# Kernel tuning notes

Hardware: AMD Instinct MI355X
Metric: run time of the kernel (lower is better)

## Reference

```python
import jax, jax.numpy as jnp
import numpy as np

N = 50000      # nodes
E = 800000     # edges (avg degree 16)
F_IN = 128
H = 128        # hidden_channels
C = 10         # num_classes
S = 5          # Chebyshev order K
B = 8          # graphs in batch


def setup_inputs() -> dict:
    key = jax.random.key(0)
    ks = jax.random.split(key, 9)
    x = jax.random.normal(ks[0], (N, F_IN), jnp.float32)
    edge_index = jax.random.randint(ks[1], (2, E), 0, N, dtype=jnp.int64)
    batch = jnp.sort(jax.random.randint(ks[2], (N,), 0, B, dtype=jnp.int64))
    lambda_max = 2.0 * jnp.ones((B,), jnp.float32)
    W1 = jax.random.normal(ks[3], (S, F_IN, H), jnp.float32) * 0.05
    b1 = jax.random.normal(ks[4], (H,), jnp.float32) * 0.05
    W2 = jax.random.normal(ks[5], (S, H, H), jnp.float32) * 0.05
    b2 = jax.random.normal(ks[6], (H,), jnp.float32) * 0.05
    Wlin = jax.random.normal(ks[7], (H, C), jnp.float32) * 0.05
    blin = jax.random.normal(ks[8], (C,), jnp.float32) * 0.05
    return {"x": x, "edge_index": edge_index, "batch": batch,
            "lambda_max": lambda_max, "W1": W1, "b1": b1,
            "W2": W2, "b2": b2, "Wlin": Wlin, "blin": blin}


def _cheb_conv(x, row, col, w_edge, diag, W, b):
    # scaled Laplacian matvec: L_hat v = scatter(w_edge * v[col] -> row) + diag * v
    def Lhat(v):
        msg = v[col] * w_edge[:, None]                       # [E, d]
        return jax.ops.segment_sum(msg, row, num_segments=N) + diag[:, None] * v

    Tx0 = x
    out = Tx0 @ W[0]
    Tx1 = Lhat(Tx0)
    out = out + Tx1 @ W[1]
    for k in range(2, W.shape[0]):                           # Chebyshev recurrence
        Tx2 = 2.0 * Lhat(Tx1) - Tx0
        out = out + Tx2 @ W[k]
        Tx0, Tx1 = Tx1, Tx2
    return out + b


def reference(x, edge_index, batch, lambda_max, W1, b1, W2, b2, Wlin, blin):
    row, col = edge_index[0], edge_index[1]
    # sym-normalized Laplacian L = I - D^{-1/2} A D^{-1/2}; L_hat = 2L/lambda_max - I
    deg = jax.ops.segment_sum(jnp.ones((E,), x.dtype), row, num_segments=N)
    dis = jnp.where(deg > 0, jax.lax.rsqrt(jnp.maximum(deg, 1e-12)), 0.0)
    lam_e = lambda_max[batch[row]]                           # per-edge lambda_max
    w_edge = -2.0 * dis[row] * dis[col] / lam_e              # off-diagonal of L_hat
    diag = 2.0 / lambda_max[batch] - 1.0                     # diagonal of L_hat per node

    h = jax.nn.relu(_cheb_conv(x, row, col, w_edge, diag, W1, b1))
    h = jax.nn.relu(_cheb_conv(h, row, col, w_edge, diag, W2, b2))

    # global_mean_pool over batch assignment
    sums = jax.ops.segment_sum(h, batch, num_segments=B)     # [B, H]
    counts = jax.ops.segment_sum(jnp.ones((N, 1), h.dtype), batch, num_segments=B)
    pooled = sums / jnp.maximum(counts, 1.0)
    return pooled @ Wlin + blin                              # [B, C] logits (softmax unused in forward)
```

## Files before the change

kernel.cpp:

```cpp
#include <hip/hip_runtime.h>
#include <hip/hip_bf16.h>
#include <stdint.h>

typedef __attribute__((ext_vector_type(8))) short bf16x8;
typedef __attribute__((ext_vector_type(4))) float f32x4;

__device__ __forceinline__ float bf16lo_to_f(uint32_t u) { return __uint_as_float(u << 16); }
__device__ __forceinline__ float bf16hi_to_f(uint32_t u) { return __uint_as_float(u & 0xffff0000u); }
__device__ __forceinline__ uint16_t f_to_bf16(float f) {
    uint32_t u = __float_as_uint(f);
    uint32_t r = u + 0x7fff + ((u >> 16) & 1);
    return (uint16_t)(r >> 16);
}


#define BINCH 4096

__global__ void __launch_bounds__(256) k_bhist(const int* __restrict__ row,
                                               int* __restrict__ bhist, int E) {
    __shared__ int sh[256];
    int t = threadIdx.x;
    sh[t] = 0;
    __syncthreads();
    int stride = gridDim.x * blockDim.x;
    for (int e = blockIdx.x * blockDim.x + t; e < E; e += stride)
        atomicAdd(&sh[row[e] >> 8], 1);
    __syncthreads();
    if (sh[t]) atomicAdd(&bhist[t], sh[t]);
}

__global__ void k_bscan(const int* __restrict__ bhist, int* __restrict__ gbase,
                        int* __restrict__ gcur, int nbk) {
    __shared__ int sh[256];
    int t = threadIdx.x;
    int v = t < nbk ? bhist[t] : 0;
    sh[t] = v;
    __syncthreads();
    for (int o = 1; o < 256; o <<= 1) {
        int u = (t >= o) ? sh[t - o] : 0;
        __syncthreads();
        sh[t] += u;
        __syncthreads();
    }
    gbase[t] = sh[t] - v;
    gcur[t] = sh[t] - v;
    if (t == 255) gbase[256] = sh[255];
}

__global__ void __launch_bounds__(256) k_bin(const int* __restrict__ row,
        const int* __restrict__ col, int* __restrict__ gcur,
        uint32_t* __restrict__ bout, int E) {
    __shared__ uint32_t stage[BINCH];
    __shared__ int hist[256], hscan[256], hcur[256], gofs[256];
    int t = threadIdx.x;
    int e0 = blockIdx.x * BINCH;
    int ecnt = min(BINCH, E - e0);
    hist[t] = 0;
    __syncthreads();
    for (int i = t; i < ecnt; i += 256)
        atomicAdd(&hist[row[e0 + i] >> 8], 1);
    __syncthreads();
    int v = hist[t];
    hscan[t] = v;
    __syncthreads();
    for (int o = 1; o < 256; o <<= 1) {
        int u = (t >= o) ? hscan[t - o] : 0;
        __syncthreads();
        hscan[t] += u;
        __syncthreads();
    }
    hcur[t] = hscan[t] - v;
    __syncthreads();
    for (int i = t; i < ecnt; i += 256) {
        int r = row[e0 + i];
        int p = atomicAdd(&hcur[r >> 8], 1);
        stage[p] = (uint32_t)(r & 255) | ((uint32_t)col[e0 + i] << 8);
    }
    __syncthreads();
    if (v > 0) gofs[t] = atomicAdd(&gcur[t], v);
    __syncthreads();
    for (int i = t; i < ecnt; i += 256) {
        int lo = 0, hi = 255;
        while (lo < hi) { int mid = (lo + hi) >> 1; if (hscan[mid] > i) hi = mid; else lo = mid + 1; }
        int b = lo;
        int local = i - (hscan[b] - hist[b]);
        bout[gofs[b] + local] = stage[i];
    }
}

__global__ void __launch_bounds__(256) k_deg2(const uint32_t* __restrict__ bout,
        const int* __restrict__ gbase, int* __restrict__ deg, int N) {
    __shared__ int cnt[256];
    int t = threadIdx.x, b = blockIdx.x;
    cnt[t] = 0;
    __syncthreads();
    int s = gbase[b], epos = gbase[b + 1];
    for (int i = s + t; i < epos; i += 256)
        atomicAdd(&cnt[bout[i] & 255], 1);
    __syncthreads();
    int n = b * 256 + t;
    if (n < N) deg[n] = cnt[t];
}

__global__ void k_psum(const int* __restrict__ deg, int* __restrict__ psum, int N) {
    __shared__ int sh[256];
    int t = threadIdx.x;
    int idx = blockIdx.x * 256 + t;
    sh[t] = idx < N ? ((deg[idx] + 7) & ~7) : 0;
    __syncthreads();
    for (int o = 128; o > 0; o >>= 1) {
        if (t < o) sh[t] += sh[t + o];
        __syncthreads();
    }
    if (t == 0) psum[blockIdx.x] = sh[0];
}

__global__ void k_scanp(const int* __restrict__ psum, int* __restrict__ poff,
                        int* __restrict__ offs, int nb, int N) {
    __shared__ int sh[256];
    int t = threadIdx.x;
    int per = (nb + 255) >> 8;
    int base = t * per;
    int s = 0;
    for (int i = 0; i < per; i++) { int idx = base + i; if (idx < nb) s += psum[idx]; }
    sh[t] = s;
    __syncthreads();
    for (int o = 1; o < 256; o <<= 1) {
        int u = (t >= o) ? sh[t - o] : 0;
        __syncthreads();
        sh[t] += u;
        __syncthreads();
    }
    int run = sh[t] - s;
    for (int i = 0; i < per; i++) {
        int idx = base + i;
        if (idx < nb) { poff[idx] = run; run += psum[idx]; }
    }
    if (t == 255) offs[N] = sh[255];
}

__global__ void k_offs(const int* __restrict__ deg, const int* __restrict__ poff,
                       int* __restrict__ offs,
                       const int* __restrict__ batch, const float* __restrict__ lam,
                       float* __restrict__ dis, float* __restrict__ diag, int N) {
    __shared__ int sh[256];
    int t = threadIdx.x;
    int idx = blockIdx.x * 256 + t;
    int d = idx < N ? deg[idx] : 0;
    int v = (d + 7) & ~7;
    sh[t] = v;
    __syncthreads();
    for (int o = 1; o < 256; o <<= 1) {
        int u = (t >= o) ? sh[t - o] : 0;
        __syncthreads();
        sh[t] += u;
        __syncthreads();
    }
    if (idx < N) {
        offs[idx] = poff[blockIdx.x] + sh[t] - v;
        dis[idx] = d > 0 ? rsqrtf((float)d) : 0.f;
        diag[idx] = 2.f / lam[batch[idx]] - 1.f;
    }
}

__global__ void __launch_bounds__(256) k_csr2(const uint32_t* __restrict__ bout,
        const int* __restrict__ gbase, const int* __restrict__ offs,
        uint16_t* __restrict__ csr, int N) {
    __shared__ int cur[256];
    int t = threadIdx.x, b = blockIdx.x;
    int n = b * 256 + t;
    cur[t] = n < N ? offs[n] : 0;
    __syncthreads();
    int s = gbase[b], epos = gbase[b + 1];
    for (int i = s + t; i < epos; i += 256) {
        uint32_t v = bout[i];
        int p = atomicAdd(&cur[v & 255], 1);
        csr[p] = (uint16_t)(v >> 8);
    }
}

__global__ void k_prepw(const float* __restrict__ W1, uint16_t* __restrict__ Wt1,
                        const float* __restrict__ W2, uint16_t* __restrict__ Wt2) {
    int i = blockIdx.x * blockDim.x + threadIdx.x;
    const float* W = W1; uint16_t* Wt = Wt1;
    if (i >= 128 * 640) { i -= 128 * 640; W = W2; Wt = Wt2; }
    int o = i / 640, kk = i % 640;
    Wt[(size_t)o * 640 + kk] = f_to_bf16(W[(size_t)kk * 128 + o]);
}

__global__ void __launch_bounds__(256) k_castx(const float* __restrict__ x,
        uint16_t* __restrict__ Txb, int8_t* __restrict__ Txq,
        const float* __restrict__ dis, float* __restrict__ mS, int N) {
    int n = (blockIdx.x * blockDim.x + threadIdx.x) >> 6;
    int lane = threadIdx.x & 63;
    if (n >= N) return;
    float2 v = ((const float2*)x)[(size_t)n * 64 + lane];
    uint32_t p = (uint32_t)f_to_bf16(v.x) | ((uint32_t)f_to_bf16(v.y) << 16);
    ((uint32_t*)Txb)[(size_t)n * 320 + lane] = p;
    float m = fmaxf(fabsf(v.x), fabsf(v.y));
    for (int o = 1; o < 64; o <<= 1) m = fmaxf(m, __shfl_xor(m, o));
    float inv = m > 0.f ? 127.f / m : 0.f;
    int qx = (int)rintf(v.x * inv), qy = (int)rintf(v.y * inv);
    uint16_t qp = (uint16_t)((qx & 0xff) | ((qy & 0xff) << 8));
    *(uint16_t*)(Txq + (size_t)n * 640 + 2 * lane) = qp;
    if (lane == 0) mS[n] = (m > 0.f ? m * (1.f / 127.f) : 0.f) * dis[n];
}

__global__ void __launch_bounds__(256) k_lhat(
        int8_t* __restrict__ Txq, uint16_t* __restrict__ Txb,
        const int* __restrict__ offs, const uint16_t* __restrict__ csr,
        const float* __restrict__ diag, const float* __restrict__ dis,
        float* __restrict__ mS, int N,
        int src, int dst, int prev, float alpha, int use_prev) {
    int n = (blockIdx.x * blockDim.x + threadIdx.x) >> 6;
    int lane = threadIdx.x & 63;
    if (n >= N) return;
    int beg = offs[n], end = offs[n + 1];
    float dgn = diag[n], dn = dis[n];
    float aS = -alpha * dn * (dgn + 1.0f);
    const float* mSrc = mS + (size_t)src * (N + 1);
    const int8_t* qbase = Txq + src * 128 + 2 * lane;
    float ax = 0.f, ay = 0.f;
    for (int e = beg; e < end; e += 8) {
        uint4 cw = *(const uint4*)(csr + e);
        int cc[8] = { (int)(cw.x & 0xffff), (int)(cw.x >> 16),
                      (int)(cw.y & 0xffff), (int)(cw.y >> 16),
                      (int)(cw.z & 0xffff), (int)(cw.z >> 16),
                      (int)(cw.w & 0xffff), (int)(cw.w >> 16) };
        float mm[8];
        uint16_t qv[8];
#pragma unroll
        for (int u = 0; u < 8; u++) mm[u] = mSrc[cc[u]];
#pragma unroll
        for (int u = 0; u < 8; u++)
            qv[u] = *(const uint16_t*)(qbase + (size_t)cc[u] * 640);
#pragma unroll
        for (int u = 0; u < 8; u++) {
            float f = aS * mm[u];
            ax = fmaf(f, (float)(int)(int8_t)(qv[u] & 0xff), ax);
            ay = fmaf(f, (float)(int)(int8_t)(qv[u] >> 8), ay);
        }
    }
    const uint32_t* bb = (const uint32_t*)Txb;
    uint32_t sv = bb[(size_t)n * 320 + src * 64 + lane];
    float ad = alpha * dgn;
    ax += ad * bf16lo_to_f(sv);
    ay += ad * bf16hi_to_f(sv);
    if (use_prev) {
        uint32_t pv = bb[(size_t)n * 320 + prev * 64 + lane];
        ax -= bf16lo_to_f(pv);
        ay -= bf16hi_to_f(pv);
    }
    uint32_t outv = (uint32_t)f_to_bf16(ax) | ((uint32_t)f_to_bf16(ay) << 16);
    ((uint32_t*)Txb)[(size_t)n * 320 + dst * 64 + lane] = outv;
    float m = fmaxf(fabsf(ax), fabsf(ay));
    for (int o = 1; o < 64; o <<= 1) m = fmaxf(m, __shfl_xor(m, o));
    float inv = m > 0.f ? 127.f / m : 0.f;
    int qx = (int)rintf(ax * inv), qy = (int)rintf(ay * inv);
    uint16_t qp = (uint16_t)((qx & 0xff) | ((qy & 0xff) << 8));
    *(uint16_t*)(Txq + (size_t)n * 640 + dst * 128 + 2 * lane) = qp;
    if (lane == 0)
        mS[(size_t)dst * (N + 1) + n] = (m > 0.f ? m * (1.f / 127.f) : 0.f) * dn;
}

#define BM 128
#define BK 64
#define LDT 72
#define LDC 132

__global__ void __launch_bounds__(256) k_gemm(
        const uint16_t* __restrict__ A, int lda,
        const uint16_t* __restrict__ Bt,
        const float* __restrict__ bias,
        uint16_t* __restrict__ out, int ldo,
        uint16_t* __restrict__ out2b,
        int8_t* __restrict__ out2q,
        const float* __restrict__ dis, float* __restrict__ mS,
        int M, int Kdim) {
    __shared__ uint16_t smem[BM * LDT + 128 * LDT];
    uint16_t* As = smem;
    uint16_t* Bs = smem + BM * LDT;
    uint16_t* Ct = smem;
    int t = threadIdx.x;
    int w = t >> 6, lane = t & 63;
    int row0 = blockIdx.x * BM;
    int mrow = (w >> 1) * 64, ncol = (w & 1) * 64;

    int ar[4], akc[4];
#pragma unroll
    for (int rep = 0; rep < 4; rep++) {
        int d = rep * 256 + t;
        ar[rep] = d >> 3; akc[rep] = d & 7;
    }

    f32x4 acc[4][4];
#pragma unroll
    for (int i = 0; i < 4; i++)
#pragma unroll
        for (int j = 0; j < 4; j++) acc[i][j] = (f32x4){0.f, 0.f, 0.f, 0.f};

    bf16x8 pa[4], pb[4];
#pragma unroll
    for (int rep = 0; rep < 4; rep++) {
        int grow = row0 + ar[rep];
        bf16x8 va = {0, 0, 0, 0, 0, 0, 0, 0};
        if (grow < M) va = *(const bf16x8*)(A + (size_t)grow * lda + akc[rep] * 8);
        pa[rep] = va;
        pb[rep] = *(const bf16x8*)(Bt + (size_t)ar[rep] * Kdim + akc[rep] * 8);
    }

    for (int k0 = 0; k0 < Kdim; k0 += BK) {
#pragma unroll
        for (int rep = 0; rep < 4; rep++) {
            *(bf16x8*)(&As[ar[rep] * LDT + akc[rep] * 8]) = pa[rep];
            *(bf16x8*)(&Bs[ar[rep] * LDT + akc[rep] * 8]) = pb[rep];
        }
        __syncthreads();
        int kn = k0 + BK;
        if (kn < Kdim) {
#pragma unroll
            for (int rep = 0; rep < 4; rep++) {
                int grow = row0 + ar[rep];
                bf16x8 va = {0, 0, 0, 0, 0, 0, 0, 0};
                if (grow < M) va = *(const bf16x8*)(A + (size_t)grow * lda + kn + akc[rep] * 8);
                pa[rep] = va;
                pb[rep] = *(const bf16x8*)(Bt + (size_t)ar[rep] * Kdim + kn + akc[rep] * 8);
            }
        }
#pragma unroll
        for (int ks = 0; ks < BK; ks += 32) {
            bf16x8 af[4], bfr[4];
#pragma unroll
            for (int i = 0; i < 4; i++) {
                int r = mrow + i * 16 + (lane & 15);
                af[i] = *(const bf16x8*)(&As[r * LDT + ks + (lane >> 4) * 8]);
            }
#pragma unroll
            for (int j = 0; j < 4; j++) {
                int c = ncol + j * 16 + (lane & 15);
                bfr[j] = *(const bf16x8*)(&Bs[c * LDT + ks + (lane >> 4) * 8]);
            }
#pragma unroll
            for (int i = 0; i < 4; i++)
#pragma unroll
                for (int j = 0; j < 4; j++)
                    acc[i][j] = __builtin_amdgcn_mfma_f32_16x16x32_bf16(af[i], bfr[j], acc[i][j], 0, 0, 0);
        }
        __syncthreads();
    }

#pragma unroll
    for (int j = 0; j < 4; j++) {
        int c = ncol + j * 16 + (lane & 15);
        float bv = bias[c];
#pragma unroll
        for (int i = 0; i < 4; i++) {
            int rloc = mrow + i * 16 + (lane >> 4) * 4;
#pragma unroll
            for (int r = 0; r < 4; r++) {
                float v = acc[i][j][r] + bv;
                v = v > 0.f ? v : 0.f;
                Ct[(rloc + r) * LDC + c] = f_to_bf16(v);
            }
        }
    }
    __syncthreads();
#pragma unroll
    for (int rep = 0; rep < 8; rep++) {
        int d = rep * 256 + t;
        int r = d >> 4, c8 = (d & 15) * 8;
        int grow = row0 + r;
        if (grow < M) {
            bf16x8 v = *(const bf16x8*)(&Ct[r * LDC + c8]);
            *(bf16x8*)(out + (size_t)grow * ldo + c8) = v;
            if (out2b) *(bf16x8*)(out2b + (size_t)grow * 640 + c8) = v;
        }
    }
    if (out2q) {
        int r = t >> 1, half = t & 1;
        int grow = row0 + r;
        float vmax = 0.f;
        for (int j = 0; j < 32; j++) {
            uint32_t u = *(const uint32_t*)(&Ct[r * LDC + half * 64 + j * 2]);
            vmax = fmaxf(vmax, fmaxf(fabsf(bf16lo_to_f(u)), fabsf(bf16hi_to_f(u))));
        }
        vmax = fmaxf(vmax, __shfl_xor(vmax, 1));
        if (grow < M) {
            float inv = vmax > 0.f ? 127.f / vmax : 0.f;
            for (int j0 = 0; j0 < 16; j0++) {
                uint32_t u0 = *(const uint32_t*)(&Ct[r * LDC + half * 64 + j0 * 4]);
                uint32_t u1 = *(const uint32_t*)(&Ct[r * LDC + half * 64 + j0 * 4 + 2]);
                int q0 = (int)rintf(bf16lo_to_f(u0) * inv);
                int q1 = (int)rintf(bf16hi_to_f(u0) * inv);
                int q2 = (int)rintf(bf16lo_to_f(u1) * inv);
                int q3 = (int)rintf(bf16hi_to_f(u1) * inv);
                uint32_t pk = (q0 & 0xff) | ((q1 & 0xff) << 8) |
                              ((q2 & 0xff) << 16) | ((uint32_t)(q3 & 0xff) << 24);
                *(uint32_t*)(out2q + (size_t)grow * 640 + half * 64 + j0 * 4) = pk;
            }
            if (half == 0)
                mS[grow] = (vmax > 0.f ? vmax * (1.f / 127.f) : 0.f) * dis[grow];
        }
    }
}

__global__ void __launch_bounds__(128) k_pool(const uint16_t* __restrict__ h,
        const int* __restrict__ batch, float* __restrict__ pooled, int N, int CH) {
    int f = threadIdx.x;
    int n0 = blockIdx.x * CH;
    if (n0 >= N) return;
    int n1 = min(n0 + CH, N);
    float acc = 0.f;
    int cur = batch[n0];
    for (int n = n0; n < n1; ++n) {
        int b = batch[n];
        if (b != cur) { atomicAdd(&pooled[cur * 128 + f], acc); acc = 0.f; cur = b; }
        acc += __uint_as_float(((uint32_t)h[(size_t)n * 128 + f]) << 16);
    }
    atomicAdd(&pooled[cur * 128 + f], acc);
}

__global__ void k_final(const float* __restrict__ pooled, const int* __restrict__ batch,
                        const float* __restrict__ Wlin, const float* __restrict__ blin,
                        float* __restrict__ out, int N, int B_, int C_) {
    __shared__ int cnt[64];
    int t = threadIdx.x;
    if (t < B_) {
        auto lb = [&](int v) {
            int lo = 0, hi = N;
            while (lo < hi) {
                int mid = (lo + hi) >> 1;
                if (batch[mid] < v) lo = mid + 1; else hi = mid;
            }
            return lo;
        };
        cnt[t] = lb(t + 1) - lb(t);
    }
    __syncthreads();
    if (t < B_ * C_) {
        int b = t / C_, c = t % C_;
        float inv = 1.f / fmaxf((float)cnt[b], 1.f);
        float acc = blin[c];
        for (int f = 0; f < 128; ++f) acc += pooled[b * 128 + f] * inv * Wlin[f * C_ + c];
        out[t] = acc;
    }
}

extern "C" void kernel_launch(void* const* d_in, const int* in_sizes, int n_in,
                              void* d_out, int out_size, void* d_ws, size_t ws_size,
                              hipStream_t stream) {
    const float* x    = (const float*)d_in[0];
    const int*   edge = (const int*)d_in[1];
    const int*   batch= (const int*)d_in[2];
    const float* lam  = (const float*)d_in[3];
    const float* W1   = (const float*)d_in[4];
    const float* b1   = (const float*)d_in[5];
    const float* W2   = (const float*)d_in[6];
    const float* b2   = (const float*)d_in[7];
    const float* Wlin = (const float*)d_in[8];
    const float* blin = (const float*)d_in[9];
    const int E  = in_sizes[1] / 2;
    const int N  = in_sizes[2];
    const int B_ = in_sizes[3];
    const int* row = edge;
    const int* col = edge + E;

    char* ws = (char*)d_ws;
    size_t off = 0;
    auto take = [&](size_t bytes) -> char* {
        char* p = ws + off;
        off = (off + bytes + 255) & ~(size_t)255;
        return p;
    };
    uint16_t* Txb    = (uint16_t*)take((size_t)N * 640 * 2);
    int8_t*   Txq    = (int8_t*)take((size_t)(N + 1) * 640);
    uint16_t* h      = (uint16_t*)take((size_t)N * 128 * 2);
    uint16_t* csr    = (uint16_t*)take(((size_t)E + 8 * (size_t)N) * 2);
    uint32_t* bout   = (uint32_t*)take((size_t)E * 4);
    float*    mS     = (float*)take((size_t)5 * (N + 1) * 4);
    int*      deg    = (int*)take((size_t)N * 4);
    int*      offs   = (int*)take((size_t)(N + 1) * 4);
    float*    dis    = (float*)take((size_t)N * 4);
    float*    diag   = (float*)take((size_t)N * 4);
    uint16_t* Wt1    = (uint16_t*)take((size_t)128 * 640 * 2);
    uint16_t* Wt2    = (uint16_t*)take((size_t)128 * 640 * 2);
    float*    pooled = (float*)take((size_t)B_ * 128 * 4);
    int*      bhist  = (int*)take(257 * 4);
    int*      gbase  = (int*)take(257 * 4);
    int*      gcur   = (int*)take(257 * 4);
    const int nb = (N + 255) / 256;
    int*      psum   = (int*)take((size_t)nb * 4);
    int*      poff   = (int*)take((size_t)nb * 4);

    hipMemsetAsync(pooled, 0, (size_t)B_ * 128 * 4, stream);
    hipMemsetAsync(mS, 0, (size_t)5 * (N + 1) * 4, stream);
    hipMemsetAsync(bhist, 0, 257 * 4, stream);
    hipMemsetD16Async((hipDeviceptr_t)csr, (unsigned short)N,
                      (size_t)E + 8 * (size_t)N, stream);

    k_bhist<<<112, 256, 0, stream>>>(row, bhist, E);
    k_bscan<<<1, 256, 0, stream>>>(bhist, gbase, gcur, nb);
    k_bin<<<(E + BINCH - 1) / BINCH, 256, 0, stream>>>(row, col, gcur, bout, E);
    k_deg2<<<nb, 256, 0, stream>>>(bout, gbase, deg, N);
    k_psum<<<nb, 256, 0, stream>>>(deg, psum, N);
    k_scanp<<<1, 256, 0, stream>>>(psum, poff, offs, nb, N);
    k_offs<<<nb, 256, 0, stream>>>(deg, poff, offs, batch, lam, dis, diag, N);
    k_csr2<<<nb, 256, 0, stream>>>(bout, gbase, offs, csr, N);
    k_prepw<<<(2 * 128 * 640) / 256, 256, 0, stream>>>(W1, Wt1, W2, Wt2);
    k_castx<<<(N + 3) / 4, 256, 0, stream>>>(x, Txb, Txq, dis, mS, N);

    const int lblocks = (N + 3) / 4;
    const int gblocks = (N + BM - 1) / BM;

    k_lhat<<<lblocks, 256, 0, stream>>>(Txq, Txb, offs, csr, diag, dis, mS, N, 0, 1, 0, 1.f, 0);
    k_lhat<<<lblocks, 256, 0, stream>>>(Txq, Txb, offs, csr, diag, dis, mS, N, 1, 2, 0, 2.f, 1);
    k_lhat<<<lblocks, 256, 0, stream>>>(Txq, Txb, offs, csr, diag, dis, mS, N, 2, 3, 1, 2.f, 1);
    k_lhat<<<lblocks, 256, 0, stream>>>(Txq, Txb, offs, csr, diag, dis, mS, N, 3, 4, 2, 2.f, 1);
    k_gemm<<<gblocks, 256, 0, stream>>>(Txb, 640, Wt1, b1, h, 128, Txb, Txq, dis, mS, N, 640);

    k_lhat<<<lblocks, 256, 0, stream>>>(Txq, Txb, offs, csr, diag, dis, mS, N, 0, 1, 0, 1.f, 0);
    k_lhat<<<lblocks, 256, 0, stream>>>(Txq, Txb, offs, csr, diag, dis, mS, N, 1, 2, 0, 2.f, 1);
    k_lhat<<<lblocks, 256, 0, stream>>>(Txq, Txb, offs, csr, diag, dis, mS, N, 2, 3, 1, 2.f, 1);
    k_lhat<<<lblocks, 256, 0, stream>>>(Txq, Txb, offs, csr, diag, dis, mS, N, 3, 4, 2, 2.f, 1);
    k_gemm<<<gblocks, 256, 0, stream>>>(Txb, 640, Wt2, b2, h, 128,
                                        (uint16_t*)nullptr, (int8_t*)nullptr, dis, mS, N, 640);

    k_pool<<<(N + 127) / 128, 128, 0, stream>>>(h, batch, pooled, N, 128);
    k_final<<<1, 128, 0, stream>>>(pooled, batch, Wlin, blin, (float*)d_out, N, B_, 10);
}
```

Measured before the change: 513.7 us.

## Cut memsets and bf16 reads in lhat, fuse degree/psum, pad CSR in-kernel

Removes the full mS and CSR memsets: only the dummy-node entries of mS are zeroed in the scan kernel, and CSR padding slots are filled by k_csr2 after its scatter. Fuses the per-block padded-degree reduction into k_deg2, dropping a launch. k_lhat now reads its self and previous Chebyshev terms from the int8 copy with a stored per-node scale instead of the bf16 copy, and writes bf16 outputs with nontemporal stores. The first GEMM no longer writes the unused h output. The int8 self/prev terms add quantization error to the recurrence, and scq is an extra per-node array.

```diff
diff --git a/kernel.cpp b/kernel.cpp
--- a/kernel.cpp
+++ b/kernel.cpp
@@ -30,7 +30,7 @@
 }
 
 __global__ void k_bscan(const int* __restrict__ bhist, int* __restrict__ gbase,
-                        int* __restrict__ gcur, int nbk) {
+                        int* __restrict__ gcur, float* __restrict__ mS, int nbk, int N) {
     __shared__ int sh[256];
     int t = threadIdx.x;
     int v = t < nbk ? bhist[t] : 0;
@@ -45,6 +45,7 @@
     gbase[t] = sh[t] - v;
     gcur[t] = sh[t] - v;
     if (t == 255) gbase[256] = sh[255];
+    if (t < 5) mS[(size_t)t * (N + 1) + N] = 0.f;
 }
 
 __global__ void __launch_bounds__(256) k_bin(const int* __restrict__ row,
@@ -89,8 +90,10 @@
 }
 
 __global__ void __launch_bounds__(256) k_deg2(const uint32_t* __restrict__ bout,
-        const int* __restrict__ gbase, int* __restrict__ deg, int N) {
+        const int* __restrict__ gbase, int* __restrict__ deg,
+        int* __restrict__ psum, int N) {
     __shared__ int cnt[256];
+    __shared__ int red[256];
     int t = threadIdx.x, b = blockIdx.x;
     cnt[t] = 0;
     __syncthreads();
@@ -99,20 +102,15 @@
         atomicAdd(&cnt[bout[i] & 255], 1);
     __syncthreads();
     int n = b * 256 + t;
-    if (n < N) deg[n] = cnt[t];
-}
-
-__global__ void k_psum(const int* __restrict__ deg, int* __restrict__ psum, int N) {
-    __shared__ int sh[256];
-    int t = threadIdx.x;
-    int idx = blockIdx.x * 256 + t;
-    sh[t] = idx < N ? ((deg[idx] + 7) & ~7) : 0;
+    int d = cnt[t];
+    if (n < N) deg[n] = d;
+    red[t] = (n < N) ? ((d + 7) & ~7) : 0;
     __syncthreads();
     for (int o = 128; o > 0; o >>= 1) {
-        if (t < o) sh[t] += sh[t + o];
-        __syncthreads();
-    }
-    if (t == 0) psum[blockIdx.x] = sh[0];
+        if (t < o) red[t] += red[t + o];
+        __syncthreads();
+    }
+    if (t == 0) psum[b] = red[0];
 }
 
 __global__ void k_scanp(const int* __restrict__ psum, int* __restrict__ poff,
@@ -169,13 +167,20 @@
     __shared__ int cur[256];
     int t = threadIdx.x, b = blockIdx.x;
     int n = b * 256 + t;
-    cur[t] = n < N ? offs[n] : 0;
+    int o0 = n < N ? offs[n] : 0;
+    cur[t] = o0;
     __syncthreads();
     int s = gbase[b], epos = gbase[b + 1];
     for (int i = s + t; i < epos; i += 256) {
         uint32_t v = bout[i];
         int p = atomicAdd(&cur[v & 255], 1);
         csr[p] = (uint16_t)(v >> 8);
+    }
+    __syncthreads();
+    if (n < N) {
+        int e = cur[t];
+        int pe = o0 + ((e - o0 + 7) & ~7);
+        for (int p = e; p < pe; p++) csr[p] = (uint16_t)N;
     }
 }
 
@@ -190,27 +195,32 @@
 
 __global__ void __launch_bounds__(256) k_castx(const float* __restrict__ x,
         uint16_t* __restrict__ Txb, int8_t* __restrict__ Txq,
-        const float* __restrict__ dis, float* __restrict__ mS, int N) {
+        const float* __restrict__ dis, float* __restrict__ mS,
+        float* __restrict__ scq, int N) {
     int n = (blockIdx.x * blockDim.x + threadIdx.x) >> 6;
     int lane = threadIdx.x & 63;
     if (n >= N) return;
     float2 v = ((const float2*)x)[(size_t)n * 64 + lane];
     uint32_t p = (uint32_t)f_to_bf16(v.x) | ((uint32_t)f_to_bf16(v.y) << 16);
-    ((uint32_t*)Txb)[(size_t)n * 320 + lane] = p;
+    __builtin_nontemporal_store(p, &((uint32_t*)Txb)[(size_t)n * 320 + lane]);
     float m = fmaxf(fabsf(v.x), fabsf(v.y));
     for (int o = 1; o < 64; o <<= 1) m = fmaxf(m, __shfl_xor(m, o));
     float inv = m > 0.f ? 127.f / m : 0.f;
     int qx = (int)rintf(v.x * inv), qy = (int)rintf(v.y * inv);
     uint16_t qp = (uint16_t)((qx & 0xff) | ((qy & 0xff) << 8));
     *(uint16_t*)(Txq + (size_t)n * 640 + 2 * lane) = qp;
-    if (lane == 0) mS[n] = (m > 0.f ? m * (1.f / 127.f) : 0.f) * dis[n];
+    if (lane == 0) {
+        float sc = m > 0.f ? m * (1.f / 127.f) : 0.f;
+        mS[n] = sc * dis[n];
+        scq[n] = sc;
+    }
 }
 
 __global__ void __launch_bounds__(256) k_lhat(
         int8_t* __restrict__ Txq, uint16_t* __restrict__ Txb,
         const int* __restrict__ offs, const uint16_t* __restrict__ csr,
         const float* __restrict__ diag, const float* __restrict__ dis,
-        float* __restrict__ mS, int N,
+        float* __restrict__ mS, float* __restrict__ scq, int N,
         int src, int dst, int prev, float alpha, int use_prev) {
     int n = (blockIdx.x * blockDim.x + threadIdx.x) >> 6;
     int lane = threadIdx.x & 63;
@@ -241,26 +251,31 @@
             ay = fmaf(f, (float)(int)(int8_t)(qv[u] >> 8), ay);
         }
     }
-    const uint32_t* bb = (const uint32_t*)Txb;
-    uint32_t sv = bb[(size_t)n * 320 + src * 64 + lane];
-    float ad = alpha * dgn;
-    ax += ad * bf16lo_to_f(sv);
-    ay += ad * bf16hi_to_f(sv);
+    {
+        uint16_t qsv = *(const uint16_t*)(Txq + (size_t)n * 640 + src * 128 + 2 * lane);
+        float ad = alpha * dgn * scq[(size_t)src * (N + 1) + n];
+        ax = fmaf(ad, (float)(int)(int8_t)(qsv & 0xff), ax);
+        ay = fmaf(ad, (float)(int)(int8_t)(qsv >> 8), ay);
+    }
     if (use_prev) {
-        uint32_t pv = bb[(size_t)n * 320 + prev * 64 + lane];
-        ax -= bf16lo_to_f(pv);
-        ay -= bf16hi_to_f(pv);
+        uint16_t qpv = *(const uint16_t*)(Txq + (size_t)n * 640 + prev * 128 + 2 * lane);
+        float sp = scq[(size_t)prev * (N + 1) + n];
+        ax = fmaf(-sp, (float)(int)(int8_t)(qpv & 0xff), ax);
+        ay = fmaf(-sp, (float)(int)(int8_t)(qpv >> 8), ay);
     }
     uint32_t outv = (uint32_t)f_to_bf16(ax) | ((uint32_t)f_to_bf16(ay) << 16);
-    ((uint32_t*)Txb)[(size_t)n * 320 + dst * 64 + lane] = outv;
+    __builtin_nontemporal_store(outv, &((uint32_t*)Txb)[(size_t)n * 320 + dst * 64 + lane]);
     float m = fmaxf(fabsf(ax), fabsf(ay));
     for (int o = 1; o < 64; o <<= 1) m = fmaxf(m, __shfl_xor(m, o));
     float inv = m > 0.f ? 127.f / m : 0.f;
     int qx = (int)rintf(ax * inv), qy = (int)rintf(ay * inv);
     uint16_t qp = (uint16_t)((qx & 0xff) | ((qy & 0xff) << 8));
     *(uint16_t*)(Txq + (size_t)n * 640 + dst * 128 + 2 * lane) = qp;
-    if (lane == 0)
-        mS[(size_t)dst * (N + 1) + n] = (m > 0.f ? m * (1.f / 127.f) : 0.f) * dn;
+    if (lane == 0) {
+        float sc = m > 0.f ? m * (1.f / 127.f) : 0.f;
+        mS[(size_t)dst * (N + 1) + n] = sc * dn;
+        scq[(size_t)dst * (N + 1) + n] = sc;
+    }
 }
 
 #define BM 128
@@ -276,6 +291,7 @@
         uint16_t* __restrict__ out2b,
         int8_t* __restrict__ out2q,
         const float* __restrict__ dis, float* __restrict__ mS,
+        float* __restrict__ scq,
         int M, int Kdim) {
     __shared__ uint16_t smem[BM * LDT + 128 * LDT];
     uint16_t* As = smem;
@@ -372,7 +388,7 @@
         int grow = row0 + r;
         if (grow < M) {
             bf16x8 v = *(const bf16x8*)(&Ct[r * LDC + c8]);
-            *(bf16x8*)(out + (size_t)grow * ldo + c8) = v;
+            if (out)   *(bf16x8*)(out + (size_t)grow * ldo + c8) = v;
             if (out2b) *(bf16x8*)(out2b + (size_t)grow * 640 + c8) = v;
         }
     }
@@ -398,8 +414,11 @@
                               ((q2 & 0xff) << 16) | ((uint32_t)(q3 & 0xff) << 24);
                 *(uint32_t*)(out2q + (size_t)grow * 640 + half * 64 + j0 * 4) = pk;
             }
-            if (half == 0)
-                mS[grow] = (vmax > 0.f ? vmax * (1.f / 127.f) : 0.f) * dis[grow];
+            if (half == 0) {
+                float sc = vmax > 0.f ? vmax * (1.f / 127.f) : 0.f;
+                mS[grow] = sc * dis[grow];
+                scq[grow] = sc;
+            }
         }
     }
 }
@@ -478,6 +497,7 @@
     uint16_t* csr    = (uint16_t*)take(((size_t)E + 8 * (size_t)N) * 2);
     uint32_t* bout   = (uint32_t*)take((size_t)E * 4);
     float*    mS     = (float*)take((size_t)5 * (N + 1) * 4);
+    float*    scq    = (float*)take((size_t)5 * (N + 1) * 4);
     int*      deg    = (int*)take((size_t)N * 4);
     int*      offs   = (int*)take((size_t)(N + 1) * 4);
     float*    dis    = (float*)take((size_t)N * 4);
@@ -493,37 +513,34 @@
     int*      poff   = (int*)take((size_t)nb * 4);
 
     hipMemsetAsync(pooled, 0, (size_t)B_ * 128 * 4, stream);
-    hipMemsetAsync(mS, 0, (size_t)5 * (N + 1) * 4, stream);
     hipMemsetAsync(bhist, 0, 257 * 4, stream);
-    hipMemsetD16Async((hipDeviceptr_t)csr, (unsigned short)N,
-                      (size_t)E + 8 * (size_t)N, stream);
 
     k_bhist<<<112, 256, 0, stream>>>(row, bhist, E);
-    k_bscan<<<1, 256, 0, stream>>>(bhist, gbase, gcur, nb);
+    k_bscan<<<1, 256, 0, stream>>>(bhist, gbase, gcur, mS, nb, N);
     k_bin<<<(E + BINCH - 1) / BINCH, 256, 0, stream>>>(row, col, gcur, bout, E);
-    k_deg2<<<nb, 256, 0, stream>>>(bout, gbase, deg, N);
-    k_psum<<<nb, 256, 0, stream>>>(deg, psum, N);
+    k_deg2<<<nb, 256, 0, stream>>>(bout, gbase, deg, psum, N);
     k_scanp<<<1, 256, 0, stream>>>(psum, poff, offs, nb, N);
     k_offs<<<nb, 256, 0, stream>>>(deg, poff, offs, batch, lam, dis, diag, N);
     k_csr2<<<nb, 256, 0, stream>>>(bout, gbase, offs, csr, N);
     k_prepw<<<(2 * 128 * 640) / 256, 256, 0, stream>>>(W1, Wt1, W2, Wt2);
-    k_castx<<<(N + 3) / 4, 256, 0, stream>>>(x, Txb, Txq, dis, mS, N);
+    k_castx<<<(N + 3) / 4, 256, 0, stream>>>(x, Txb, Txq, dis, mS, scq, N);
 
     const int lblocks = (N + 3) / 4;
     const int gblocks = (N + BM - 1) / BM;
 
-    k_lhat<<<lblocks, 256, 0, stream>>>(Txq, Txb, offs, csr, diag, dis, mS, N, 0, 1, 0, 1.f, 0);
-    k_lhat<<<lblocks, 256, 0, stream>>>(Txq, Txb, offs, csr, diag, dis, mS, N, 1, 2, 0, 2.f, 1);
-    k_lhat<<<lblocks, 256, 0, stream>>>(Txq, Txb, offs, csr, diag, dis, mS, N, 2, 3, 1, 2.f, 1);
-    k_lhat<<<lblocks, 256, 0, stream>>>(Txq, Txb, offs, csr, diag, dis, mS, N, 3, 4, 2, 2.f, 1);
-    k_gemm<<<gblocks, 256, 0, stream>>>(Txb, 640, Wt1, b1, h, 128, Txb, Txq, dis, mS, N, 640);
-
-    k_lhat<<<lblocks, 256, 0, stream>>>(Txq, Txb, offs, csr, diag, dis, mS, N, 0, 1, 0, 1.f, 0);
-    k_lhat<<<lblocks, 256, 0, stream>>>(Txq, Txb, offs, csr, diag, dis, mS, N, 1, 2, 0, 2.f, 1);
-    k_lhat<<<lblocks, 256, 0, stream>>>(Txq, Txb, offs, csr, diag, dis, mS, N, 2, 3, 1, 2.f, 1);
-    k_lhat<<<lblocks, 256, 0, stream>>>(Txq, Txb, offs, csr, diag, dis, mS, N, 3, 4, 2, 2.f, 1);
+    k_lhat<<<lblocks, 256, 0, stream>>>(Txq, Txb, offs, csr, diag, dis, mS, scq, N, 0, 1, 0, 1.f, 0);
+    k_lhat<<<lblocks, 256, 0, stream>>>(Txq, Txb, offs, csr, diag, dis, mS, scq, N, 1, 2, 0, 2.f, 1);
+    k_lhat<<<lblocks, 256, 0, stream>>>(Txq, Txb, offs, csr, diag, dis, mS, scq, N, 2, 3, 1, 2.f, 1);
+    k_lhat<<<lblocks, 256, 0, stream>>>(Txq, Txb, offs, csr, diag, dis, mS, scq, N, 3, 4, 2, 2.f, 1);
+    k_gemm<<<gblocks, 256, 0, stream>>>(Txb, 640, Wt1, b1,
+                                        (uint16_t*)nullptr, 128, Txb, Txq, dis, mS, scq, N, 640);
+
+    k_lhat<<<lblocks, 256, 0, stream>>>(Txq, Txb, offs, csr, diag, dis, mS, scq, N, 0, 1, 0, 1.f, 0);
+    k_lhat<<<lblocks, 256, 0, stream>>>(Txq, Txb, offs, csr, diag, dis, mS, scq, N, 1, 2, 0, 2.f, 1);
+    k_lhat<<<lblocks, 256, 0, stream>>>(Txq, Txb, offs, csr, diag, dis, mS, scq, N, 2, 3, 1, 2.f, 1);
+    k_lhat<<<lblocks, 256, 0, stream>>>(Txq, Txb, offs, csr, diag, dis, mS, scq, N, 3, 4, 2, 2.f, 1);
     k_gemm<<<gblocks, 256, 0, stream>>>(Txb, 640, Wt2, b2, h, 128,
-                                        (uint16_t*)nullptr, (int8_t*)nullptr, dis, mS, N, 640);
+                                        (uint16_t*)nullptr, (int8_t*)nullptr, dis, mS, scq, N, 640);
 
     k_pool<<<(N + 127) / 128, 128, 0, stream>>>(h, batch, pooled, N, 128);
     k_final<<<1, 128, 0, stream>>>(pooled, batch, Wlin, blin, (float*)d_out, N, B_, 10);
```

Result: no change. 513.5 us (-0.0%).
